# Kernel optimization log

Hardware: AMD Instinct MI355X
Metric: run time of the kernel (lower is better)

## Reference

```python
import jax, jax.numpy as jnp
import numpy as np

T, B, V, E, H, L = 128, 32, 50000, 512, 512, 2


def _lstm_layer(x, h0, c0, Wih, Whh, bih, bhh):
    # x: [T, B, in]; torch gate order i, f, g, o
    def step(carry, xt):
        h, c = carry
        gates = xt @ Wih.T + bih + h @ Whh.T + bhh  # [B, 4H]
        i, f, g, o = jnp.split(gates, 4, axis=-1)
        c = jax.nn.sigmoid(f) * c + jax.nn.sigmoid(i) * jnp.tanh(g)
        h = jax.nn.sigmoid(o) * jnp.tanh(c)
        return (h, c), h
    (h, c), ys = jax.lax.scan(step, (h0, c0), x)
    return ys, h, c


def setup_inputs() -> dict:
    key = jax.random.key(0)
    ks = jax.random.split(key, 12)
    s = 0.02
    return {
        'word': jax.random.randint(ks[0], (B,), 0, V),
        'seq': jax.random.randint(ks[1], (T, B), 0, V),
        'emb': jax.random.normal(ks[2], (V, E), jnp.float32) * s,
        'w2h_W': jax.random.normal(ks[3], (H, E), jnp.float32) * s,
        'w2h_b': jnp.zeros((H,), jnp.float32),
        'Wih0': jax.random.normal(ks[4], (4 * H, E), jnp.float32) * s,
        'Whh0': jax.random.normal(ks[5], (4 * H, H), jnp.float32) * s,
        'bih0': jnp.zeros((4 * H,), jnp.float32),
        'bhh0': jnp.zeros((4 * H,), jnp.float32),
        'Wih1': jax.random.normal(ks[6], (4 * H, H), jnp.float32) * s,
        'Whh1': jax.random.normal(ks[7], (4 * H, H), jnp.float32) * s,
        'bih1': jnp.zeros((4 * H,), jnp.float32),
        'bhh1': jnp.zeros((4 * H,), jnp.float32),
        'dec_W': jax.random.normal(ks[8], (V, H), jnp.float32) * s,
        'dec_b': jnp.zeros((V,), jnp.float32),
    }


def reference(word, seq, emb, w2h_W, w2h_b, Wih0, Whh0, bih0, bhh0,
              Wih1, Whh1, bih1, bhh1, dec_W, dec_b):
    word_emb = emb[word]                       # [B, E]
    seq_emb = emb[seq]                         # [T, B, E] (dropouts are 0/eval)
    # init_hidden: c0 = word2hidden(word_emb) expanded to all layers, h0 = 0
    c0 = word_emb @ w2h_W.T + w2h_b            # [B, H]
    h0 = jnp.zeros_like(c0)
    # 2-layer LSTM; stepping all layers per timestep == running layers sequentially
    y0, h_f0, c_f0 = _lstm_layer(seq_emb, h0, c0, Wih0, Whh0, bih0, bhh0)
    y1, h_f1, c_f1 = _lstm_layer(y0, h0, c0, Wih1, Whh1, bih1, bhh1)
    out = y1.reshape(T * B, H)                 # [T*B, H]
    decoded = out @ dec_W.T + dec_b            # [T*B, V]
    h_final = jnp.stack([h_f0, h_f1], axis=0)  # [L, B, H]
    c_final = jnp.stack([c_f0, c_f1], axis=0)
    return decoded, h_final, c_final
```

## Files before the change

### kernel.cpp

```cpp
#include <hip/hip_runtime.h>
#include <hip/hip_bf16.h>
#include <cstdint>

#define T_STEPS 128
#define BATCH   32
#define VOCAB   50000
#define EDIM    512
#define HDIM    512
#define GDIM    2048
#define MROWS   4096
#define VPAD    50048
#define BH      (BATCH * HDIM)

typedef short bf16x8 __attribute__((ext_vector_type(8)));
typedef float f32x4  __attribute__((ext_vector_type(4)));
typedef unsigned short us4 __attribute__((ext_vector_type(4)));
typedef unsigned short us8 __attribute__((ext_vector_type(8)));

#define MFMA16(a, b, c) __builtin_amdgcn_mfma_f32_16x16x32_bf16(a, b, c, 0, 0, 0)

__device__ __forceinline__ float fsigmoid(float x) { return 1.0f / (1.0f + __expf(-x)); }
__device__ __forceinline__ float ftanh(float x)    { return 1.0f - 2.0f / (1.0f + __expf(2.0f * x)); }

__device__ __forceinline__ unsigned short f2bf(float f) {
    unsigned int u = __float_as_uint(f);
    u = (u + 0x7fffu + ((u >> 16) & 1u)) >> 16;
    return (unsigned short)u;
}


__global__ __launch_bounds__(64) void pack_all(const float* __restrict__ s0,
                                               const float* __restrict__ s1,
                                               const float* __restrict__ s2,
                                               const float* __restrict__ s3,
                                               unsigned short* __restrict__ d0,
                                               unsigned short* __restrict__ d1,
                                               unsigned short* __restrict__ d2,
                                               unsigned short* __restrict__ d3) {
    const int which = blockIdx.x >> 11;
    const int n = blockIdx.x & 2047;
    const float* src = (which == 0) ? s0 : (which == 1) ? s1 : (which == 2) ? s2 : s3;
    unsigned short* dst = (which == 0) ? d0 : (which == 1) ? d1 : (which == 2) ? d2 : d3;
    const int orig = (n & 3) * 512 + (n >> 2);
    const int k = threadIdx.x * 8;
    const float* s = src + (long)orig * 512 + k;
    float4 a = *(const float4*)s;
    float4 b = *(const float4*)(s + 4);
    us8 v;
    v[0] = f2bf(a.x); v[1] = f2bf(a.y); v[2] = f2bf(a.z); v[3] = f2bf(a.w);
    v[4] = f2bf(b.x); v[5] = f2bf(b.y); v[6] = f2bf(b.z); v[7] = f2bf(b.w);
    *(us8*)(dst + (long)n * 512 + k) = v;
}

__global__ __launch_bounds__(256) void pack_bias(const float* __restrict__ bih0,
                                                 const float* __restrict__ bhh0,
                                                 const float* __restrict__ bih1,
                                                 const float* __restrict__ bhh1,
                                                 float* __restrict__ b0p,
                                                 float* __restrict__ b1p) {
    const int n = blockIdx.x * 256 + threadIdx.x;
    const int orig = (n & 3) * 512 + (n >> 2);
    b0p[n] = bih0[orig] + bhh0[orig];
    b1p[n] = bih1[orig] + bhh1[orig];
}

__global__ __launch_bounds__(256) void gather_x(const int* __restrict__ seq,
                                                const float* __restrict__ emb,
                                                unsigned short* __restrict__ Xbf) {
    long i = ((long)blockIdx.x * 256 + threadIdx.x) * 4;
    if (i >= (long)MROWS * EDIM) return;
    int r   = (int)(i >> 9);
    int col = (int)(i & 511);
    const float* er = emb + (long)seq[r] * EDIM + col;
    float4 e = *(const float4*)er;
    us4 v;
    v[0] = f2bf(e.x); v[1] = f2bf(e.y); v[2] = f2bf(e.z); v[3] = f2bf(e.w);
    *(us4*)(Xbf + i) = v;
}

__global__ __launch_bounds__(256) void init_c0(const int* __restrict__ word,
                                               const float* __restrict__ emb,
                                               const float* __restrict__ w2hW,
                                               const float* __restrict__ w2hb,
                                               float* __restrict__ c0s, float* __restrict__ c1s,
                                               unsigned short* __restrict__ y0bf,
                                               unsigned short* __restrict__ y1bf) {
    const int idx = blockIdx.x * 256 + threadIdx.x;
    const int b = idx >> 9, hh = idx & 511;
    const float* er = emb + (long)word[b] * EDIM;
    const float* wr = w2hW + (long)hh * EDIM;
    float acc = w2hb[hh];
    #pragma unroll 4
    for (int k = 0; k < EDIM; k += 4) {
        float4 e4 = *(const float4*)(er + k);
        float4 w4 = *(const float4*)(wr + k);
        acc += e4.x * w4.x + e4.y * w4.y + e4.z * w4.z + e4.w * w4.w;
    }
    c0s[idx] = acc;
    c1s[idx] = acc;
    y0bf[idx] = 0;
    y1bf[idx] = 0;
}

__global__ __launch_bounds__(512, 4) void gemm_bt256(const unsigned short* __restrict__ A,
                                                     const unsigned short* __restrict__ Bt,
                                                     float* __restrict__ C,
                                                     const float* __restrict__ bias1,
                                                     int K, int Nreal, long ldc, int ntn,
                                                     const float* __restrict__ cvsrc,
                                                     unsigned short* __restrict__ cvdst,
                                                     int ngemm) {
    const int tid = threadIdx.x;
    if (blockIdx.x >= ngemm) {
        long i = ((long)(blockIdx.x - ngemm) * 512 + tid) * 8;
        if (i >= (long)VPAD * EDIM) return;
        long row = i >> 9;
        us8 v;
        if (row < VOCAB) {
            float4 a = *(const float4*)(cvsrc + i);
            float4 b = *(const float4*)(cvsrc + i + 4);
            v[0] = f2bf(a.x); v[1] = f2bf(a.y); v[2] = f2bf(a.z); v[3] = f2bf(a.w);
            v[4] = f2bf(b.x); v[5] = f2bf(b.y); v[6] = f2bf(b.z); v[7] = f2bf(b.w);
        } else {
            v = (us8)0;
        }
        *(us8*)(cvdst + i) = v;
        return;
    }

    __shared__ __align__(16) unsigned char smem[49152];
    unsigned short* As = (unsigned short*)smem;
    unsigned short* Bs = (unsigned short*)(smem + 32768);
    float* ctile = (float*)smem;

    const long m0  = (long)(blockIdx.x / ntn) * 256;
    const long n0  = (long)(blockIdx.x % ntn) * 128;
    const int lane = tid & 63;
    const int wave = tid >> 6;
    const int wr = wave >> 1, wc = wave & 1;
    const int fr = lane & 15, fq = lane >> 4;
    const int srow = tid >> 3;
    const int scol = (tid & 7) * 8;

    f32x4 acc[4][4];
    #pragma unroll
    for (int i = 0; i < 4; ++i)
        #pragma unroll
        for (int j = 0; j < 4; ++j) acc[i][j] = (f32x4)0.0f;

    for (int kt = 0; kt < K; kt += 64) {
        #pragma unroll
        for (int i = 0; i < 4; ++i) {
            const unsigned short* ga = A + (m0 + i * 64 + srow) * K + kt + scol;
            __builtin_amdgcn_global_load_lds((const __attribute__((address_space(1))) void*)ga,
                                             (__attribute__((address_space(3))) void*)(As + i * 4096 + tid * 8),
                                             16, 0, 0);
        }
        #pragma unroll
        for (int i = 0; i < 2; ++i) {
            const unsigned short* gb = Bt + (n0 + i * 64 + srow) * K + kt + scol;
            __builtin_amdgcn_global_load_lds((const __attribute__((address_space(1))) void*)gb,
                                             (__attribute__((address_space(3))) void*)(Bs + i * 4096 + tid * 8),
                                             16, 0, 0);
        }
        asm volatile("s_waitcnt vmcnt(0)" ::: "memory");
        __syncthreads();
        #pragma unroll
        for (int ks = 0; ks < 64; ks += 32) {
            bf16x8 af[4], bfr[4];
            #pragma unroll
            for (int mi = 0; mi < 4; ++mi)
                af[mi] = *(const bf16x8*)&As[(wr * 64 + mi * 16 + fr) * 64 + ks + fq * 8];
            #pragma unroll
            for (int ni = 0; ni < 4; ++ni)
                bfr[ni] = *(const bf16x8*)&Bs[(wc * 64 + ni * 16 + fr) * 64 + ks + fq * 8];
            #pragma unroll
            for (int mi = 0; mi < 4; ++mi)
                #pragma unroll
                for (int ni = 0; ni < 4; ++ni)
                    acc[mi][ni] = MFMA16(af[mi], bfr[ni], acc[mi][ni]);
        }
        __syncthreads();
    }

    #pragma unroll
    for (int h = 0; h < 4; ++h) {
        if (wr == h) {
            #pragma unroll
            for (int ni = 0; ni < 4; ++ni) {
                const long col = n0 + wc * 64 + ni * 16 + fr;
                float bs = (col < Nreal && bias1) ? bias1[col] : 0.0f;
                #pragma unroll
                for (int mi = 0; mi < 4; ++mi)
                    #pragma unroll
                    for (int r = 0; r < 4; ++r)
                        ctile[(mi * 16 + fq * 4 + r) * 132 + wc * 64 + ni * 16 + fr] =
                            acc[mi][ni][r] + bs;
            }
        }
        __syncthreads();
        #pragma unroll
        for (int j = 0; j < 4; ++j) {
            const int flat = tid + j * 512;
            const int row = flat >> 5, colq = flat & 31;
            const long col4 = n0 + colq * 4;
            if (col4 < Nreal) {
                f32x4 v = *(const f32x4*)&ctile[row * 132 + colq * 4];
                *(f32x4*)&C[(m0 + h * 64 + row) * ldc + col4] = v;
            }
        }
        __syncthreads();
    }
}

__global__ __launch_bounds__(512) void lstm_step2(
        const float* __restrict__ G0,
        const unsigned short* __restrict__ Whh0p,
        const unsigned short* __restrict__ Wih1p,
        const unsigned short* __restrict__ Whh1p,
        const float* __restrict__ b1p,
        unsigned short* __restrict__ y0bf,
        unsigned short* __restrict__ y1bf,
        float* __restrict__ c0s, float* __restrict__ c1s,
        float* __restrict__ hf,
        int t) {
    __shared__ float part[8][32][32];
    int bid = blockIdx.x;
    const int tid  = threadIdx.x;
    const int wv   = tid >> 6, lane = tid & 63;
    const int fr   = lane & 15, fq = lane >> 4;

    int layer, tt, cg;
    if (bid < 64) { layer = 0; tt = t;     if (tt >= T_STEPS) return; cg = bid; }
    else          { layer = 1; tt = t - 1; if (tt < 0) return;       cg = bid - 64; }

    const unsigned short* hin;
    unsigned short* yout;
    float* cs;
    if (layer == 0) { hin = y0bf + (long)tt * BH; yout = y0bf + (long)(tt + 1) * BH; cs = c0s; }
    else            { hin = y1bf + (long)tt * BH; yout = y1bf + (long)(tt + 1) * BH; cs = c1s; }

    const int n_base = cg * 32;

    const int pb = tid >> 3, pu = tid & 7;
    const int si = pb * HDIM + cg * 8 + pu;
    float creg = 0.0f;
    float4 ad = make_float4(0.f, 0.f, 0.f, 0.f);
    if (tid < 256) {
        creg = cs[si];
        if (layer == 0) ad = *(const float4*)(G0 + ((long)tt * BATCH + pb) * GDIM + n_base + pu * 4);
        else            ad = *(const float4*)(b1p + n_base + pu * 4);
    }

    f32x4 acc[2][2];
    acc[0][0] = (f32x4)0.0f; acc[0][1] = (f32x4)0.0f;
    acc[1][0] = (f32x4)0.0f; acc[1][1] = (f32x4)0.0f;

    if (layer == 0) {
        const int kbase = wv * 64;
        const unsigned short* A0 = hin + fr * 512 + kbase + fq * 8;
        const unsigned short* A1 = A0 + 16 * 512;
        const unsigned short* B0 = Whh0p + (long)(n_base + fr) * 512 + kbase + fq * 8;
        const unsigned short* B1 = B0 + 16 * 512;
        #pragma unroll
        for (int i = 0; i < 2; ++i) {
            bf16x8 a0 = *(const bf16x8*)(A0 + i * 32);
            bf16x8 a1 = *(const bf16x8*)(A1 + i * 32);
            bf16x8 b0 = *(const bf16x8*)(B0 + i * 32);
            bf16x8 b1 = *(const bf16x8*)(B1 + i * 32);
            acc[0][0] = MFMA16(a0, b0, acc[0][0]);
            acc[0][1] = MFMA16(a0, b1, acc[0][1]);
            acc[1][0] = MFMA16(a1, b0, acc[1][0]);
            acc[1][1] = MFMA16(a1, b1, acc[1][1]);
        }
    } else {
        const unsigned short* Aop = (wv < 4) ? (y0bf + (long)(tt + 1) * BH) : hin;
        const unsigned short* Bop = (wv < 4) ? Wih1p : Whh1p;
        const int kbase = (wv & 3) * 128;
        const unsigned short* A0 = Aop + fr * 512 + kbase + fq * 8;
        const unsigned short* A1 = A0 + 16 * 512;
        const unsigned short* B0 = Bop + (long)(n_base + fr) * 512 + kbase + fq * 8;
        const unsigned short* B1 = B0 + 16 * 512;
        #pragma unroll
        for (int i = 0; i < 4; ++i) {
            bf16x8 a0 = *(const bf16x8*)(A0 + i * 32);
            bf16x8 a1 = *(const bf16x8*)(A1 + i * 32);
            bf16x8 b0 = *(const bf16x8*)(B0 + i * 32);
            bf16x8 b1 = *(const bf16x8*)(B1 + i * 32);
            acc[0][0] = MFMA16(a0, b0, acc[0][0]);
            acc[0][1] = MFMA16(a0, b1, acc[0][1]);
            acc[1][0] = MFMA16(a1, b0, acc[1][0]);
            acc[1][1] = MFMA16(a1, b1, acc[1][1]);
        }
    }

    #pragma unroll
    for (int mi = 0; mi < 2; ++mi)
        #pragma unroll
        for (int ni = 0; ni < 2; ++ni)
            #pragma unroll
            for (int r = 0; r < 4; ++r)
                part[wv][mi * 16 + fq * 4 + r][ni * 16 + fr] = acc[mi][ni][r];
    __syncthreads();

    if (tid < 256) {
        float4 g4 = *(const float4*)&part[0][pb][pu * 4];
        #pragma unroll
        for (int w = 1; w < 8; ++w) {
            float4 p4 = *(const float4*)&part[w][pb][pu * 4];
            g4.x += p4.x; g4.y += p4.y; g4.z += p4.z; g4.w += p4.w;
        }
        const float vi = g4.x + ad.x, vf = g4.y + ad.y;
        const float vg = g4.z + ad.z, vo = g4.w + ad.w;
        float c = fsigmoid(vf) * creg + fsigmoid(vi) * ftanh(vg);
        float h = fsigmoid(vo) * ftanh(c);
        cs[si] = c;
        yout[si] = f2bf(h);
        if (tt == T_STEPS - 1) hf[layer * BH + si] = h;
    }
}

__global__ __launch_bounds__(256) void finalize_states(const float* __restrict__ hf,
                                                       const float* __restrict__ c0s,
                                                       const float* __restrict__ c1s,
                                                       float* __restrict__ out) {
    const int idx = blockIdx.x * 256 + threadIdx.x;
    const long base = (long)MROWS * VOCAB;
    float v;
    if (idx < 32768)      v = hf[idx];
    else if (idx < 49152) v = c0s[idx - 32768];
    else                  v = c1s[idx - 49152];
    out[base + idx] = v;
}

extern "C" void kernel_launch(void* const* d_in, const int* in_sizes, int n_in,
                              void* d_out, int out_size, void* d_ws, size_t ws_size,
                              hipStream_t stream) {
    const int*   word  = (const int*)d_in[0];
    const int*   seq   = (const int*)d_in[1];
    const float* emb   = (const float*)d_in[2];
    const float* w2hW  = (const float*)d_in[3];
    const float* w2hb  = (const float*)d_in[4];
    const float* Wih0  = (const float*)d_in[5];
    const float* Whh0  = (const float*)d_in[6];
    const float* bih0  = (const float*)d_in[7];
    const float* bhh0  = (const float*)d_in[8];
    const float* Wih1  = (const float*)d_in[9];
    const float* Whh1  = (const float*)d_in[10];
    const float* bih1  = (const float*)d_in[11];
    const float* bhh1  = (const float*)d_in[12];
    const float* dec_W = (const float*)d_in[13];
    const float* dec_b = (const float*)d_in[14];
    float* out = (float*)d_out;

    char* ws = (char*)d_ws;
    size_t off = 0;
    float*          G0    = (float*)(ws + off);          off += (size_t)MROWS * GDIM * 4;
    unsigned short* Xbf   = (unsigned short*)(ws + off); off += (size_t)MROWS * EDIM * 2;
    unsigned short* Wih0p = (unsigned short*)(ws + off); off += (size_t)GDIM  * EDIM * 2;
    unsigned short* Whh0p = (unsigned short*)(ws + off); off += (size_t)GDIM  * HDIM * 2;
    unsigned short* Wih1p = (unsigned short*)(ws + off); off += (size_t)GDIM  * HDIM * 2;
    unsigned short* Whh1p = (unsigned short*)(ws + off); off += (size_t)GDIM  * HDIM * 2;
    unsigned short* decWb = (unsigned short*)(ws + off); off += (size_t)VPAD  * EDIM * 2;
    unsigned short* y0bf  = (unsigned short*)(ws + off); off += (size_t)(T_STEPS + 1) * BH * 2;
    unsigned short* y1bf  = (unsigned short*)(ws + off); off += (size_t)(T_STEPS + 1) * BH * 2;
    float* b0p = (float*)(ws + off); off += (size_t)GDIM * 4;
    float* b1p = (float*)(ws + off); off += (size_t)GDIM * 4;
    float* c0s = (float*)(ws + off); off += (size_t)BH * 4;
    float* c1s = (float*)(ws + off); off += (size_t)BH * 4;
    float* hf  = (float*)(ws + off); off += (size_t)2 * BH * 4;

    pack_all<<<4 * 2048, 64, 0, stream>>>(Wih0, Whh0, Wih1, Whh1,
                                          Wih0p, Whh0p, Wih1p, Whh1p);
    pack_bias<<<8, 256, 0, stream>>>(bih0, bhh0, bih1, bhh1, b0p, b1p);
    gather_x<<<2048, 256, 0, stream>>>(seq, emb, Xbf);
    init_c0<<<64, 256, 0, stream>>>(word, emb, w2hW, w2hb, c0s, c1s, y0bf, y1bf);

    gemm_bt256<<<256 + 6256, 512, 0, stream>>>(Xbf, Wih0p, G0, b0p,
                                               512, GDIM, (long)GDIM, 16,
                                               dec_W, decWb, 256);

    for (int t = 0; t <= T_STEPS; ++t)
        lstm_step2<<<128, 512, 0, stream>>>(G0, Whh0p, Wih1p, Whh1p, b1p,
                                            y0bf, y1bf, c0s, c1s, hf, t);

    gemm_bt256<<<16 * 391, 512, 0, stream>>>(y1bf + BH, decWb, out, dec_b,
                                             512, VOCAB, (long)VOCAB, 391,
                                             nullptr, nullptr, 16 * 391);

    finalize_states<<<256, 256, 0, stream>>>(hf, c0s, c1s, out);
}
```

Measured before the change: 1.259 ms.

## Merge init kernels into one launch and enlarge GEMM tile to 512 rows

Combines the four setup kernels (weight packing, bias packing, embedding gather, c0 init) into one launch to cut launch overhead. The GEMM moves to 1024-thread blocks covering 512x128 tiles, so each B tile is reused across twice as many rows and the block count halves. In exchange it uses 80KB of LDS per block and larger blocks, which lowers occupancy and can leave some CUs idle on the input-projection GEMM (only 128 blocks).

```diff
diff --git a/kernel.cpp b/kernel.cpp
--- a/kernel.cpp
+++ b/kernel.cpp
@@ -28,91 +28,78 @@
     return (unsigned short)u;
 }
 
-
-__global__ __launch_bounds__(64) void pack_all(const float* __restrict__ s0,
-                                               const float* __restrict__ s1,
-                                               const float* __restrict__ s2,
-                                               const float* __restrict__ s3,
-                                               unsigned short* __restrict__ d0,
-                                               unsigned short* __restrict__ d1,
-                                               unsigned short* __restrict__ d2,
-                                               unsigned short* __restrict__ d3) {
-    const int which = blockIdx.x >> 11;
-    const int n = blockIdx.x & 2047;
-    const float* src = (which == 0) ? s0 : (which == 1) ? s1 : (which == 2) ? s2 : s3;
-    unsigned short* dst = (which == 0) ? d0 : (which == 1) ? d1 : (which == 2) ? d2 : d3;
-    const int orig = (n & 3) * 512 + (n >> 2);
-    const int k = threadIdx.x * 8;
-    const float* s = src + (long)orig * 512 + k;
-    float4 a = *(const float4*)s;
-    float4 b = *(const float4*)(s + 4);
-    us8 v;
-    v[0] = f2bf(a.x); v[1] = f2bf(a.y); v[2] = f2bf(a.z); v[3] = f2bf(a.w);
-    v[4] = f2bf(b.x); v[5] = f2bf(b.y); v[6] = f2bf(b.z); v[7] = f2bf(b.w);
-    *(us8*)(dst + (long)n * 512 + k) = v;
-}
-
-__global__ __launch_bounds__(256) void pack_bias(const float* __restrict__ bih0,
-                                                 const float* __restrict__ bhh0,
-                                                 const float* __restrict__ bih1,
-                                                 const float* __restrict__ bhh1,
-                                                 float* __restrict__ b0p,
-                                                 float* __restrict__ b1p) {
-    const int n = blockIdx.x * 256 + threadIdx.x;
-    const int orig = (n & 3) * 512 + (n >> 2);
-    b0p[n] = bih0[orig] + bhh0[orig];
-    b1p[n] = bih1[orig] + bhh1[orig];
-}
-
-__global__ __launch_bounds__(256) void gather_x(const int* __restrict__ seq,
-                                                const float* __restrict__ emb,
-                                                unsigned short* __restrict__ Xbf) {
-    long i = ((long)blockIdx.x * 256 + threadIdx.x) * 4;
-    if (i >= (long)MROWS * EDIM) return;
-    int r   = (int)(i >> 9);
-    int col = (int)(i & 511);
-    const float* er = emb + (long)seq[r] * EDIM + col;
-    float4 e = *(const float4*)er;
-    us4 v;
-    v[0] = f2bf(e.x); v[1] = f2bf(e.y); v[2] = f2bf(e.z); v[3] = f2bf(e.w);
-    *(us4*)(Xbf + i) = v;
-}
-
-__global__ __launch_bounds__(256) void init_c0(const int* __restrict__ word,
-                                               const float* __restrict__ emb,
-                                               const float* __restrict__ w2hW,
-                                               const float* __restrict__ w2hb,
-                                               float* __restrict__ c0s, float* __restrict__ c1s,
-                                               unsigned short* __restrict__ y0bf,
-                                               unsigned short* __restrict__ y1bf) {
-    const int idx = blockIdx.x * 256 + threadIdx.x;
-    const int b = idx >> 9, hh = idx & 511;
-    const float* er = emb + (long)word[b] * EDIM;
-    const float* wr = w2hW + (long)hh * EDIM;
-    float acc = w2hb[hh];
-    #pragma unroll 4
-    for (int k = 0; k < EDIM; k += 4) {
-        float4 e4 = *(const float4*)(er + k);
-        float4 w4 = *(const float4*)(wr + k);
-        acc += e4.x * w4.x + e4.y * w4.y + e4.z * w4.z + e4.w * w4.w;
-    }
-    c0s[idx] = acc;
-    c1s[idx] = acc;
-    y0bf[idx] = 0;
-    y1bf[idx] = 0;
-}
-
-__global__ __launch_bounds__(512, 4) void gemm_bt256(const unsigned short* __restrict__ A,
-                                                     const unsigned short* __restrict__ Bt,
-                                                     float* __restrict__ C,
-                                                     const float* __restrict__ bias1,
-                                                     int K, int Nreal, long ldc, int ntn,
-                                                     const float* __restrict__ cvsrc,
-                                                     unsigned short* __restrict__ cvdst,
-                                                     int ngemm) {
+__global__ __launch_bounds__(256) void init_all(
+        const int* __restrict__ word, const int* __restrict__ seq,
+        const float* __restrict__ emb,
+        const float* __restrict__ w2hW, const float* __restrict__ w2hb,
+        const float* __restrict__ s0, const float* __restrict__ s1,
+        const float* __restrict__ s2, const float* __restrict__ s3,
+        unsigned short* __restrict__ d0, unsigned short* __restrict__ d1,
+        unsigned short* __restrict__ d2, unsigned short* __restrict__ d3,
+        const float* __restrict__ bih0, const float* __restrict__ bhh0,
+        const float* __restrict__ bih1, const float* __restrict__ bhh1,
+        float* __restrict__ b0p, float* __restrict__ b1p,
+        unsigned short* __restrict__ Xbf,
+        float* __restrict__ c0s, float* __restrict__ c1s,
+        unsigned short* __restrict__ y0bf, unsigned short* __restrict__ y1bf) {
+    const int bid = blockIdx.x, tid = threadIdx.x;
+    if (bid < 2048) {
+        const int which = tid >> 6;
+        const float* src = (which == 0) ? s0 : (which == 1) ? s1 : (which == 2) ? s2 : s3;
+        unsigned short* dst = (which == 0) ? d0 : (which == 1) ? d1 : (which == 2) ? d2 : d3;
+        const int orig = (bid & 3) * 512 + (bid >> 2);
+        const int k = (tid & 63) * 8;
+        const float* s = src + (long)orig * 512 + k;
+        float4 a = *(const float4*)s;
+        float4 b = *(const float4*)(s + 4);
+        us8 v;
+        v[0] = f2bf(a.x); v[1] = f2bf(a.y); v[2] = f2bf(a.z); v[3] = f2bf(a.w);
+        v[4] = f2bf(b.x); v[5] = f2bf(b.y); v[6] = f2bf(b.z); v[7] = f2bf(b.w);
+        *(us8*)(dst + (long)bid * 512 + k) = v;
+    } else if (bid < 2056) {
+        const int n = (bid - 2048) * 256 + tid;
+        const int orig = (n & 3) * 512 + (n >> 2);
+        b0p[n] = bih0[orig] + bhh0[orig];
+        b1p[n] = bih1[orig] + bhh1[orig];
+    } else if (bid < 4104) {
+        long i = ((long)(bid - 2056) * 256 + tid) * 4;
+        int r   = (int)(i >> 9);
+        int col = (int)(i & 511);
+        const float* er = emb + (long)seq[r] * EDIM + col;
+        float4 e = *(const float4*)er;
+        us4 v;
+        v[0] = f2bf(e.x); v[1] = f2bf(e.y); v[2] = f2bf(e.z); v[3] = f2bf(e.w);
+        *(us4*)(Xbf + i) = v;
+    } else {
+        const int idx = (bid - 4104) * 256 + tid;
+        const int b = idx >> 9, hh = idx & 511;
+        const float* er = emb + (long)word[b] * EDIM;
+        const float* wr = w2hW + (long)hh * EDIM;
+        float acc = w2hb[hh];
+        #pragma unroll 4
+        for (int k = 0; k < EDIM; k += 4) {
+            float4 e4 = *(const float4*)(er + k);
+            float4 w4 = *(const float4*)(wr + k);
+            acc += e4.x * w4.x + e4.y * w4.y + e4.z * w4.z + e4.w * w4.w;
+        }
+        c0s[idx] = acc;
+        c1s[idx] = acc;
+        y0bf[idx] = 0;
+        y1bf[idx] = 0;
+    }
+}
+
+__global__ __launch_bounds__(1024, 4) void gemm_bt512(const unsigned short* __restrict__ A,
+                                                      const unsigned short* __restrict__ Bt,
+                                                      float* __restrict__ C,
+                                                      const float* __restrict__ bias1,
+                                                      int K, int Nreal, long ldc, int ntn,
+                                                      const float* __restrict__ cvsrc,
+                                                      unsigned short* __restrict__ cvdst,
+                                                      int ngemm) {
     const int tid = threadIdx.x;
     if (blockIdx.x >= ngemm) {
-        long i = ((long)(blockIdx.x - ngemm) * 512 + tid) * 8;
+        long i = ((long)(blockIdx.x - ngemm) * 1024 + tid) * 8;
         if (i >= (long)VPAD * EDIM) return;
         long row = i >> 9;
         us8 v;
@@ -128,19 +115,17 @@
         return;
     }
 
-    __shared__ __align__(16) unsigned char smem[49152];
+    __shared__ __align__(16) unsigned char smem[81920];
     unsigned short* As = (unsigned short*)smem;
-    unsigned short* Bs = (unsigned short*)(smem + 32768);
+    unsigned short* Bs = (unsigned short*)(smem + 65536);
     float* ctile = (float*)smem;
 
-    const long m0  = (long)(blockIdx.x / ntn) * 256;
+    const long m0  = (long)(blockIdx.x / ntn) * 512;
     const long n0  = (long)(blockIdx.x % ntn) * 128;
     const int lane = tid & 63;
     const int wave = tid >> 6;
     const int wr = wave >> 1, wc = wave & 1;
     const int fr = lane & 15, fq = lane >> 4;
-    const int srow = tid >> 3;
-    const int scol = (tid & 7) * 8;
 
     f32x4 acc[4][4];
     #pragma unroll
@@ -149,18 +134,19 @@
         for (int j = 0; j < 4; ++j) acc[i][j] = (f32x4)0.0f;
 
     for (int kt = 0; kt < K; kt += 64) {
+        const int srow = tid >> 3;
+        const int scol = (tid & 7) * 8;
         #pragma unroll
         for (int i = 0; i < 4; ++i) {
-            const unsigned short* ga = A + (m0 + i * 64 + srow) * K + kt + scol;
+            const unsigned short* ga = A + (m0 + i * 128 + srow) * K + kt + scol;
             __builtin_amdgcn_global_load_lds((const __attribute__((address_space(1))) void*)ga,
-                                             (__attribute__((address_space(3))) void*)(As + i * 4096 + tid * 8),
+                                             (__attribute__((address_space(3))) void*)(As + i * 8192 + tid * 8),
                                              16, 0, 0);
         }
-        #pragma unroll
-        for (int i = 0; i < 2; ++i) {
-            const unsigned short* gb = Bt + (n0 + i * 64 + srow) * K + kt + scol;
+        {
+            const unsigned short* gb = Bt + (n0 + srow) * K + kt + scol;
             __builtin_amdgcn_global_load_lds((const __attribute__((address_space(1))) void*)gb,
-                                             (__attribute__((address_space(3))) void*)(Bs + i * 4096 + tid * 8),
+                                             (__attribute__((address_space(3))) void*)(Bs + tid * 8),
                                              16, 0, 0);
         }
         asm volatile("s_waitcnt vmcnt(0)" ::: "memory");
@@ -184,7 +170,7 @@
     }
 
     #pragma unroll
-    for (int h = 0; h < 4; ++h) {
+    for (int h = 0; h < 8; ++h) {
         if (wr == h) {
             #pragma unroll
             for (int ni = 0; ni < 4; ++ni) {
@@ -200,8 +186,8 @@
         }
         __syncthreads();
         #pragma unroll
-        for (int j = 0; j < 4; ++j) {
-            const int flat = tid + j * 512;
+        for (int j = 0; j < 2; ++j) {
+            const int flat = tid + j * 1024;
             const int row = flat >> 5, colq = flat & 31;
             const long col4 = n0 + colq * 4;
             if (col4 < Nreal) {
@@ -370,23 +356,23 @@
     float* c1s = (float*)(ws + off); off += (size_t)BH * 4;
     float* hf  = (float*)(ws + off); off += (size_t)2 * BH * 4;
 
-    pack_all<<<4 * 2048, 64, 0, stream>>>(Wih0, Whh0, Wih1, Whh1,
-                                          Wih0p, Whh0p, Wih1p, Whh1p);
-    pack_bias<<<8, 256, 0, stream>>>(bih0, bhh0, bih1, bhh1, b0p, b1p);
-    gather_x<<<2048, 256, 0, stream>>>(seq, emb, Xbf);
-    init_c0<<<64, 256, 0, stream>>>(word, emb, w2hW, w2hb, c0s, c1s, y0bf, y1bf);
-
-    gemm_bt256<<<256 + 6256, 512, 0, stream>>>(Xbf, Wih0p, G0, b0p,
-                                               512, GDIM, (long)GDIM, 16,
-                                               dec_W, decWb, 256);
+    init_all<<<4168, 256, 0, stream>>>(word, seq, emb, w2hW, w2hb,
+                                       Wih0, Whh0, Wih1, Whh1,
+                                       Wih0p, Whh0p, Wih1p, Whh1p,
+                                       bih0, bhh0, bih1, bhh1, b0p, b1p,
+                                       Xbf, c0s, c1s, y0bf, y1bf);
+
+    gemm_bt512<<<128 + 3128, 1024, 0, stream>>>(Xbf, Wih0p, G0, b0p,
+                                                512, GDIM, (long)GDIM, 16,
+                                                dec_W, decWb, 128);
 
     for (int t = 0; t <= T_STEPS; ++t)
         lstm_step2<<<128, 512, 0, stream>>>(G0, Whh0p, Wih1p, Whh1p, b1p,
                                             y0bf, y1bf, c0s, c1s, hf, t);
 
-    gemm_bt256<<<16 * 391, 512, 0, stream>>>(y1bf + BH, decWb, out, dec_b,
+    gemm_bt512<<<8 * 391, 1024, 0, stream>>>(y1bf + BH, decWb, out, dec_b,
                                              512, VOCAB, (long)VOCAB, 391,
-                                             nullptr, nullptr, 16 * 391);
+                                             nullptr, nullptr, 8 * 391);
 
     finalize_states<<<256, 256, 0, stream>>>(hf, c0s, c1s, out);
 }
```

After: 1.388 ms. +10.3%, slower.
